# Performance work log

Hardware: AMD Instinct MI355X
Metric: run time of the kernel (lower is better)

## Reference

```python
import math
import jax, jax.numpy as jnp
import numpy as np

B, S, D = 4, 2048, 1024
N_HEAD = 16


def setup_inputs() -> dict:
    key = jax.random.key(0)
    k1, k2 = jax.random.split(key)
    x = jax.random.normal(k1, (B, S, D), dtype=jnp.float32)
    # xavier-uniform style scale for the fused QKV kernel
    limit = math.sqrt(6.0 / (D + 3 * D))
    W_qkv = jax.random.uniform(k2, (D, 3 * D), dtype=jnp.float32, minval=-limit, maxval=limit)
    b_qkv = jnp.zeros((3 * D,), dtype=jnp.float32)
    return {"x": x, "W_qkv": W_qkv, "b_qkv": b_qkv}


def reference(x, W_qkv, b_qkv):
    batch_size, seq_len, d_model = x.shape
    head_dim = d_model // N_HEAD
    # fused QKV projection: [B, S, 3D]
    qkv = jnp.einsum('bsd,de->bse', x, W_qkv) + b_qkv
    qkv = qkv.reshape(batch_size, seq_len, N_HEAD, 3 * head_dim)
    qkv = qkv.transpose(0, 2, 1, 3)  # [B, H, S, 3*hd]
    q, k, v = jnp.split(qkv, 3, axis=-1)
    # scaled dot-product attention with causal mask
    attn_logits = jnp.einsum('bhqd,bhkd->bhqk', q, k) / math.sqrt(head_dim)
    causal = jnp.tril(jnp.ones((seq_len, seq_len), dtype=jnp.float32))[None, None]
    attn_logits = jnp.where(causal == 0, -jnp.inf, attn_logits)
    attn = jax.nn.softmax(attn_logits, axis=-1)
    out = jnp.einsum('bhqk,bhkd->bhqd', attn, v)  # [B, H, S, hd]
    out = out.transpose(0, 2, 1, 3).reshape(batch_size, seq_len, -1)
    return out
```

## Files before the change

### kernel.cpp

```cpp
#include <hip/hip_runtime.h>
#include <hip/hip_bf16.h>
#include <cstdint>

typedef __bf16 bf16x8 __attribute__((ext_vector_type(8)));
typedef float f32x16 __attribute__((ext_vector_type(16)));

__device__ inline unsigned short f2bf(float f) {
    union { float f; unsigned int u; } v; v.f = f;
    unsigned int u = v.u;
    unsigned int r = (u + 0x7FFFu + ((u >> 16) & 1u)) >> 16;
    return (unsigned short)r;
}

__device__ inline f32x16 mfma32(bf16x8 a, bf16x8 b, f32x16 c) {
    return __builtin_amdgcn_mfma_f32_32x32x16_bf16(a, b, c, 0, 0, 0);
}

__device__ inline bf16x8 ldfrag(const unsigned short* p) {
    uint4 v = *(const uint4*)p;
    return __builtin_bit_cast(bf16x8, v);
}

__device__ inline void cp16(const unsigned short* g, unsigned short* l) {
    __builtin_amdgcn_global_load_lds(
        (const __attribute__((address_space(1))) unsigned int*)g,
        (__attribute__((address_space(3))) unsigned int*)l,
        16, 0, 0);
}

__device__ inline unsigned int pkbf(float a, float b) {
    return __builtin_amdgcn_perm(__builtin_bit_cast(unsigned int, b),
                                 __builtin_bit_cast(unsigned int, a),
                                 0x07060302u);
}

__device__ inline void plswap(unsigned int& a, unsigned int& b) {
    typedef unsigned int u32x2 __attribute__((ext_vector_type(2)));
    u32x2 r = __builtin_amdgcn_permlane32_swap(a, b, false, false);
    a = r[0]; b = r[1];
}

__global__ __launch_bounds__(256) void k_prep(
    const float* __restrict__ x, unsigned short* __restrict__ xbf,
    const float* __restrict__ W, unsigned short* __restrict__ Wt) {
    __shared__ float tile[32][33];
    if (blockIdx.x < 8192) {
        int i = blockIdx.x * 256 + threadIdx.x;
        float4 f = ((const float4*)x)[i];
        ushort4 o;
        o.x = f2bf(f.x); o.y = f2bf(f.y); o.z = f2bf(f.z); o.w = f2bf(f.w);
        ((ushort4*)xbf)[i] = o;
    } else {
        int bid = blockIdx.x - 8192;
        int nt = bid % 96, kt = bid / 96;
        int tx = threadIdx.x & 31, ty = threadIdx.x >> 5;
#pragma unroll
        for (int yy = 0; yy < 4; ++yy) {
            int y = ty + yy * 8;
            tile[y][tx] = W[(size_t)(kt * 32 + y) * 3072 + nt * 32 + tx];
        }
        __syncthreads();
#pragma unroll
        for (int yy = 0; yy < 4; ++yy) {
            int nrow = ty + yy * 8;
            Wt[(size_t)(nt * 32 + nrow) * 1024 + kt * 32 + tx] =
                f2bf(tile[tx][nrow]);
        }
    }
}

__global__ __launch_bounds__(512, 2) void k_qkv_gemm(
    const unsigned short* __restrict__ A,
    const unsigned short* __restrict__ Bt,
    const float* __restrict__ bias,
    unsigned short* __restrict__ C) {
    __shared__ __align__(16) unsigned short As[3 * 256 * 64];
    __shared__ __align__(16) unsigned short Bs[3 * 128 * 64];
    const int tid = threadIdx.x;
    const int lane = tid & 63;
    const int w = tid >> 6;
    const int wm = w >> 1, wn = w & 1;
    const int l31 = lane & 31;
    const int hi = lane >> 5;
    const int xr7 = l31 & 7;
    const int m0 = blockIdx.y * 256;
    const int n0 = blockIdx.x * 128;
    const int b = blockIdx.y >> 3;

    const int srow = tid >> 3, sseg = tid & 7;
    const int gsw = (sseg ^ (srow & 7)) * 8;
    const unsigned short* pA = A + (size_t)(m0 + srow) * 1024 + gsw;
    const unsigned short* pB = Bt + (size_t)(n0 + srow) * 1024 + gsw;

    f32x16 acc[2][2] = {};

    auto stage = [&](int buf, int k0) {
        unsigned short* da = &As[buf * 16384 + tid * 8];
        unsigned short* db = &Bs[buf * 8192 + tid * 8];
#pragma unroll
        for (int i = 0; i < 4; ++i)
            cp16(pA + (size_t)i * 64 * 1024 + k0, da + i * 4096);
#pragma unroll
        for (int j = 0; j < 2; ++j)
            cp16(pB + (size_t)j * 64 * 1024 + k0, db + j * 4096);
    };

    stage(0, 0);
    stage(1, 64);

    for (int kt = 0; kt < 16; ++kt) {
        const int buf = kt % 3;
        if (kt == 15)
            asm volatile("s_waitcnt vmcnt(0)" ::: "memory");
        else
            asm volatile("s_waitcnt vmcnt(6)" ::: "memory");
        __builtin_amdgcn_s_barrier();
        if (kt + 2 < 16) stage((kt + 2) % 3, (kt + 2) * 64);

        const unsigned short* ab = &As[buf * 16384];
        const unsigned short* bb = &Bs[buf * 8192];
        bf16x8 af[2][4], bfr[2][4];
#pragma unroll
        for (int rb = 0; rb < 2; ++rb) {
            const int r = wm * 64 + rb * 32 + l31;
#pragma unroll
            for (int ks = 0; ks < 4; ++ks)
                af[rb][ks] = ldfrag(ab + r * 64 + ((ks * 2 + hi) ^ xr7) * 8);
        }
#pragma unroll
        for (int cb = 0; cb < 2; ++cb) {
            const int r = wn * 64 + cb * 32 + l31;
#pragma unroll
            for (int ks = 0; ks < 4; ++ks)
                bfr[cb][ks] = ldfrag(bb + r * 64 + ((ks * 2 + hi) ^ xr7) * 8);
        }
#pragma unroll
        for (int rb = 0; rb < 2; ++rb)
#pragma unroll
            for (int cb = 0; cb < 2; ++cb)
#pragma unroll
                for (int ks = 0; ks < 4; ++ks)
                    acc[rb][cb] = mfma32(af[rb][ks], bfr[cb][ks], acc[rb][cb]);

        asm volatile("s_waitcnt lgkmcnt(0)" ::: "memory");
    }

    const int colbase = n0 + wn * 64;
    const int seg = colbase % 192;
    const bool isV = seg == 128;
    const float scl = (seg == 0) ? 0.18033688011112042f : 1.0f;
    const int vh = colbase / 192;
    const size_t cbase = (size_t)b * 2048 * 3072;
#pragma unroll
    for (int cb = 0; cb < 2; ++cb) {
        const int col = colbase + cb * 32 + l31;
        const float bv = bias[col];
#pragma unroll
        for (int rb = 0; rb < 2; ++rb) {
            const int rbase = m0 + wm * 64 + rb * 32 + 4 * hi;
            if (isV) {
                const int d = cb * 32 + l31;
#pragma unroll
                for (int g = 0; g < 4; ++g) {
                    const int s0 = (rbase + g * 8) & 2047;
                    unsigned int lo = (unsigned int)f2bf(acc[rb][cb][g * 4 + 0] + bv) |
                                      ((unsigned int)f2bf(acc[rb][cb][g * 4 + 1] + bv) << 16);
                    unsigned int hi2 = (unsigned int)f2bf(acc[rb][cb][g * 4 + 2] + bv) |
                                       ((unsigned int)f2bf(acc[rb][cb][g * 4 + 3] + bv) << 16);
                    uint2 pk; pk.x = lo; pk.y = hi2;
                    *(uint2*)(C + cbase + (size_t)(d * 32 + (s0 >> 6)) * 3072 +
                              vh * 192 + 128 + (s0 & 63)) = pk;
                }
            } else {
#pragma unroll
                for (int g = 0; g < 4; ++g)
#pragma unroll
                    for (int rr = 0; rr < 4; ++rr) {
                        const int row = rbase + g * 8 + rr;
                        C[(size_t)row * 3072 + col] =
                            f2bf((acc[rb][cb][g * 4 + rr] + bv) * scl);
                    }
            }
        }
    }
}

__global__ __launch_bounds__(256) void k_attn(
    const unsigned short* __restrict__ qkv,
    float* __restrict__ out) {
    const int p = blockIdx.x;
    const int hb = p & 63;
    const int h = hb & 15;
    const int b = hb >> 4;
    const int qt = 31 - (p >> 6);
    const int tid = threadIdx.x;
    const int lane = tid & 63;
    const int w = tid >> 6;
    const int wm = w >> 1;
    const int wn = w & 1;
    const int l31 = lane & 31;
    const int hi = lane >> 5;

    __shared__ __align__(16) unsigned short KsF[2 * 64 * 64];
    __shared__ __align__(16) unsigned short VsF[2 * 64 * 64];

    const size_t base = (size_t)b * 2048 * 3072;
    const int qoff = h * 192, koff = h * 192 + 64, voff = h * 192 + 128;

    const int srow0 = tid >> 3, sseg = tid & 7;
    const int gsw = (sseg ^ (srow0 & 7)) * 8;
    unsigned short* kd0 = &KsF[tid * 8];
    unsigned short* kd1 = &KsF[2048 + tid * 8];
    unsigned short* vd0 = &VsF[tid * 8];
    unsigned short* vd1 = &VsF[2048 + tid * 8];

    const int xr7 = l31 & 7;
    const int kfbase = (32 * wm + l31) * 64;
    const int vfb0 = l31 * 64;
    const int vfb1 = (32 + l31) * 64;
    const int qcol = 32 * wn + l31;

    const int qrow = qt * 64 + qcol;
    const unsigned short* qp = qkv + base + (size_t)qrow * 3072 + qoff + hi * 8;
    bf16x8 bq[4];
#pragma unroll
    for (int t = 0; t < 4; ++t) bq[t] = ldfrag(qp + t * 16);

    const unsigned short* kp0 = qkv + base + koff + (size_t)srow0 * 3072 + gsw;
    const unsigned short* kp1 = kp0 + (size_t)32 * 3072;
    const unsigned short* vp0 = qkv + base + (size_t)(srow0 * 32) * 3072 + voff + gsw;
    const unsigned short* vp1 = vp0 + (size_t)1024 * 3072;

    f32x16 acc0 = {0,0,0,0,0,0,0,0,0,0,0,0,0,0,0,0};
    f32x16 acc1 = {0,0,0,0,0,0,0,0,0,0,0,0,0,0,0,0};
    float ptot = 0.f;

    cp16(kp0, kd0); cp16(kp1, kd1); cp16(vp0, vd0); cp16(vp1, vd1);
    __syncthreads();

    for (int kt = 0; kt <= qt; ++kt) {
        const int bo = (kt & 1) * 4096;
        const int bn = bo ^ 4096;
        if (kt < qt) {
            kp0 += 64 * 3072; kp1 += 64 * 3072;
            vp0 += 3072;      vp1 += 3072;
            cp16(kp0, kd0 + bn); cp16(kp1, kd1 + bn);
            cp16(vp0, vd0 + bn); cp16(vp1, vd1 + bn);
        }

        f32x16 s = {0,0,0,0,0,0,0,0,0,0,0,0,0,0,0,0};
#pragma unroll
        for (int t = 0; t < 4; ++t) {
            const unsigned short* ka =
                &KsF[bo + kfbase + ((2 * t + hi) ^ xr7) * 8];
            s = mfma32(ldfrag(ka), bq[t], s);
        }

        if (kt == qt) {
#pragma unroll
            for (int r = 0; r < 16; ++r) {
                const int srow = 32 * wm + (r & 3) + 8 * (r >> 2) + 4 * hi;
                if (srow > qcol) s[r] = -3.0e38f;
            }
        }

        float pvv[16];
#pragma unroll
        for (int r = 0; r < 16; ++r) {
            pvv[r] = __builtin_amdgcn_exp2f(s[r]);
            ptot += pvv[r];
        }
        unsigned int pk0 = pkbf(pvv[0], pvv[1]),   pk1 = pkbf(pvv[2], pvv[3]);
        unsigned int pk2 = pkbf(pvv[4], pvv[5]),   pk3 = pkbf(pvv[6], pvv[7]);
        unsigned int pk4 = pkbf(pvv[8], pvv[9]),   pk5 = pkbf(pvv[10], pvv[11]);
        unsigned int pk6 = pkbf(pvv[12], pvv[13]), pk7 = pkbf(pvv[14], pvv[15]);
        plswap(pk0, pk2); plswap(pk1, pk3);
        plswap(pk4, pk6); plswap(pk5, pk7);
        uint4 w0; w0.x = pk0; w0.y = pk1; w0.z = pk2; w0.w = pk3;
        uint4 w1; w1.x = pk4; w1.y = pk5; w1.z = pk6; w1.w = pk7;
        const bf16x8 pf0 = __builtin_bit_cast(bf16x8, w0);
        const bf16x8 pf1 = __builtin_bit_cast(bf16x8, w1);

        const int su0 = ((4 * wm + hi) ^ xr7) * 8;
        const int su1 = ((4 * wm + 2 + hi) ^ xr7) * 8;
        acc0 = mfma32(ldfrag(&VsF[bo + vfb0 + su0]), pf0, acc0);
        acc0 = mfma32(ldfrag(&VsF[bo + vfb0 + su1]), pf1, acc0);
        acc1 = mfma32(ldfrag(&VsF[bo + vfb1 + su0]), pf0, acc1);
        acc1 = mfma32(ldfrag(&VsF[bo + vfb1 + su1]), pf1, acc1);

        __syncthreads();
    }

    float* Sc = (float*)KsF;
    float* Pt = (float*)VsF;
    const int lb = (wn * 64 + lane) * 8;
    if (wm == 1) {
#pragma unroll
        for (int g = 0; g < 4; ++g) {
            float4 v;
            v.x = acc0[g * 4 + 0]; v.y = acc0[g * 4 + 1];
            v.z = acc0[g * 4 + 2]; v.w = acc0[g * 4 + 3];
            ((float4*)Sc)[lb + (g ^ (lane & 7))] = v;
        }
#pragma unroll
        for (int g = 0; g < 4; ++g) {
            float4 v;
            v.x = acc1[g * 4 + 0]; v.y = acc1[g * 4 + 1];
            v.z = acc1[g * 4 + 2]; v.w = acc1[g * 4 + 3];
            ((float4*)Sc)[lb + ((g + 4) ^ (lane & 7))] = v;
        }
        Pt[wn * 64 + lane] = ptot;
    }
    __syncthreads();
    if (wm == 0) {
#pragma unroll
        for (int g = 0; g < 4; ++g) {
            float4 v = ((const float4*)Sc)[lb + (g ^ (lane & 7))];
            acc0[g * 4 + 0] += v.x; acc0[g * 4 + 1] += v.y;
            acc0[g * 4 + 2] += v.z; acc0[g * 4 + 3] += v.w;
        }
#pragma unroll
        for (int g = 0; g < 4; ++g) {
            float4 v = ((const float4*)Sc)[lb + ((g + 4) ^ (lane & 7))];
            acc1[g * 4 + 0] += v.x; acc1[g * 4 + 1] += v.y;
            acc1[g * 4 + 2] += v.z; acc1[g * 4 + 3] += v.w;
        }
        float l = ptot + Pt[wn * 64 + lane];
        l += __shfl_xor(l, 32, 64);
        const float inv = __builtin_amdgcn_rcpf(l);
        float* op = out + ((size_t)b * 2048 + qrow) * 1024 + h * 64 + 4 * hi;
#pragma unroll
        for (int g = 0; g < 4; ++g) {
            float4 v;
            v.x = acc0[g * 4 + 0] * inv; v.y = acc0[g * 4 + 1] * inv;
            v.z = acc0[g * 4 + 2] * inv; v.w = acc0[g * 4 + 3] * inv;
            *(float4*)(op + g * 8) = v;
        }
#pragma unroll
        for (int g = 0; g < 4; ++g) {
            float4 v;
            v.x = acc1[g * 4 + 0] * inv; v.y = acc1[g * 4 + 1] * inv;
            v.z = acc1[g * 4 + 2] * inv; v.w = acc1[g * 4 + 3] * inv;
            *(float4*)(op + 32 + g * 8) = v;
        }
    }
}

extern "C" void kernel_launch(void* const* d_in, const int* in_sizes, int n_in,
                              void* d_out, int out_size, void* d_ws, size_t ws_size,
                              hipStream_t stream) {
    const float* x = (const float*)d_in[0];
    const float* W = (const float*)d_in[1];
    const float* bq = (const float*)d_in[2];
    float* out = (float*)d_out;

    unsigned short* xbf = (unsigned short*)d_ws;
    unsigned short* wtbf = xbf + (size_t)8192 * 1024;
    unsigned short* qkvbf = wtbf + (size_t)3072 * 1024;

    k_prep<<<8192 + 3072, 256, 0, stream>>>(x, xbf, W, wtbf);
    k_qkv_gemm<<<dim3(24, 32), 512, 0, stream>>>(xbf, wtbf, bq, qkvbf);
    k_attn<<<2048, 256, 0, stream>>>(qkvbf, out);
}
```

Before: 205.0 us.

## Interleave QKV GEMM LDS loads, async copies and MFMA in four sub-phases

Restructures the K-loop of the QKV projection GEMM into four phases. Each phase loads one A or B fragment set from LDS, issues half of the next tile's global-to-LDS copies, then runs one 32x32 MFMA block at raised wave priority (s_setprio), with barriers between phases. The aim is to overlap LDS reads, global prefetch and matrix math across waves, in the style of a ping-pong schedule. The cost is many extra barriers per iteration, and the vmcnt waits must stay matched to the new ordering of copies.

```diff
diff --git a/kernel.cpp b/kernel.cpp
--- a/kernel.cpp
+++ b/kernel.cpp
@@ -94,55 +94,86 @@
 
     f32x16 acc[2][2] = {};
 
-    auto stage = [&](int buf, int k0) {
+    auto stage_h1 = [&](int buf, int k0) {
         unsigned short* da = &As[buf * 16384 + tid * 8];
         unsigned short* db = &Bs[buf * 8192 + tid * 8];
-#pragma unroll
-        for (int i = 0; i < 4; ++i)
-            cp16(pA + (size_t)i * 64 * 1024 + k0, da + i * 4096);
-#pragma unroll
-        for (int j = 0; j < 2; ++j)
-            cp16(pB + (size_t)j * 64 * 1024 + k0, db + j * 4096);
+        cp16(pA + k0, da);
+        cp16(pA + (size_t)64 * 1024 + k0, da + 4096);
+        cp16(pB + k0, db);
     };
-
-    stage(0, 0);
-    stage(1, 64);
+    auto stage_h2 = [&](int buf, int k0) {
+        unsigned short* da = &As[buf * 16384 + tid * 8];
+        unsigned short* db = &Bs[buf * 8192 + tid * 8];
+        cp16(pA + (size_t)128 * 1024 + k0, da + 8192);
+        cp16(pA + (size_t)192 * 1024 + k0, da + 12288);
+        cp16(pB + (size_t)64 * 1024 + k0, db + 4096);
+    };
+
+    stage_h1(0, 0);  stage_h2(0, 0);
+    stage_h1(1, 64); stage_h2(1, 64);
+    asm volatile("s_waitcnt vmcnt(6)" ::: "memory");
+    __builtin_amdgcn_s_barrier();
 
     for (int kt = 0; kt < 16; ++kt) {
         const int buf = kt % 3;
-        if (kt == 15)
-            asm volatile("s_waitcnt vmcnt(0)" ::: "memory");
-        else
-            asm volatile("s_waitcnt vmcnt(6)" ::: "memory");
-        __builtin_amdgcn_s_barrier();
-        if (kt + 2 < 16) stage((kt + 2) % 3, (kt + 2) * 64);
-
+        const int nb = (kt + 2) % 3;
+        const int nk = (kt + 2) * 64;
         const unsigned short* ab = &As[buf * 16384];
         const unsigned short* bb = &Bs[buf * 8192];
-        bf16x8 af[2][4], bfr[2][4];
-#pragma unroll
-        for (int rb = 0; rb < 2; ++rb) {
-            const int r = wm * 64 + rb * 32 + l31;
-#pragma unroll
-            for (int ks = 0; ks < 4; ++ks)
-                af[rb][ks] = ldfrag(ab + r * 64 + ((ks * 2 + hi) ^ xr7) * 8);
-        }
-#pragma unroll
-        for (int cb = 0; cb < 2; ++cb) {
-            const int r = wn * 64 + cb * 32 + l31;
-#pragma unroll
-            for (int ks = 0; ks < 4; ++ks)
-                bfr[cb][ks] = ldfrag(bb + r * 64 + ((ks * 2 + hi) ^ xr7) * 8);
-        }
-#pragma unroll
-        for (int rb = 0; rb < 2; ++rb)
-#pragma unroll
-            for (int cb = 0; cb < 2; ++cb)
-#pragma unroll
-                for (int ks = 0; ks < 4; ++ks)
-                    acc[rb][cb] = mfma32(af[rb][ks], bfr[cb][ks], acc[rb][cb]);
-
-        asm volatile("s_waitcnt lgkmcnt(0)" ::: "memory");
+        const int ra0 = wm * 64 + l31;
+        const int ra1 = wm * 64 + 32 + l31;
+        const int rb0 = wn * 64 + l31;
+        const int rb1 = wn * 64 + 32 + l31;
+        bf16x8 af0[4], af1[4], bf0[4], bf1[4];
+
+#pragma unroll
+        for (int ks = 0; ks < 4; ++ks) {
+            af0[ks] = ldfrag(ab + ra0 * 64 + ((ks * 2 + hi) ^ xr7) * 8);
+            bf0[ks] = ldfrag(bb + rb0 * 64 + ((ks * 2 + hi) ^ xr7) * 8);
+        }
+        if (kt < 14) stage_h1(nb, nk);
+        __builtin_amdgcn_s_barrier();
+        __builtin_amdgcn_s_setprio(1);
+#pragma unroll
+        for (int ks = 0; ks < 4; ++ks)
+            acc[0][0] = mfma32(af0[ks], bf0[ks], acc[0][0]);
+        __builtin_amdgcn_s_setprio(0);
+        __builtin_amdgcn_s_barrier();
+
+#pragma unroll
+        for (int ks = 0; ks < 4; ++ks)
+            bf1[ks] = ldfrag(bb + rb1 * 64 + ((ks * 2 + hi) ^ xr7) * 8);
+        if (kt < 14) stage_h2(nb, nk);
+        __builtin_amdgcn_s_barrier();
+        __builtin_amdgcn_s_setprio(1);
+#pragma unroll
+        for (int ks = 0; ks < 4; ++ks)
+            acc[0][1] = mfma32(af0[ks], bf1[ks], acc[0][1]);
+        __builtin_amdgcn_s_setprio(0);
+        __builtin_amdgcn_s_barrier();
+
+#pragma unroll
+        for (int ks = 0; ks < 4; ++ks)
+            af1[ks] = ldfrag(ab + ra1 * 64 + ((ks * 2 + hi) ^ xr7) * 8);
+        __builtin_amdgcn_s_barrier();
+        __builtin_amdgcn_s_setprio(1);
+#pragma unroll
+        for (int ks = 0; ks < 4; ++ks)
+            acc[1][1] = mfma32(af1[ks], bf1[ks], acc[1][1]);
+        __builtin_amdgcn_s_setprio(0);
+        __builtin_amdgcn_s_barrier();
+
+        if (kt < 14)
+            asm volatile("s_waitcnt vmcnt(6)" ::: "memory");
+        else
+            asm volatile("s_waitcnt vmcnt(0)" ::: "memory");
+        __builtin_amdgcn_s_barrier();
+        __builtin_amdgcn_s_setprio(1);
+#pragma unroll
+        for (int ks = 0; ks < 4; ++ks)
+            acc[1][0] = mfma32(af1[ks], bf0[ks], acc[1][0]);
+        __builtin_amdgcn_s_setprio(0);
+        __builtin_amdgcn_s_barrier();
     }
 
     const int colbase = n0 + wn * 64;
```

New measurement: 214.8 us. 4.8% more time.
